# Performance work log

Measured on AMD Instinct MI355X. Metric: run time of the kernel, lower is better.

## Reference

```python
import jax, jax.numpy as jnp
import numpy as np

B, P, IN_DIM, OUT_DIM = 4, 120000, 4, 64
SPATIAL = (480, 360, 32)
EPS = 1e-5
SLOPE = 0.01  # LeakyReLU default negative slope


def setup_inputs() -> dict:
    key = jax.random.key(0)
    ks = jax.random.split(key, 10)
    pc = jax.random.normal(ks[0], (B, P, IN_DIM), dtype=jnp.float32)
    pc_indices = jax.random.randint(ks[1], (B, P, 3), 0, 32, dtype=jnp.int32)
    W1 = jax.random.normal(ks[2], (IN_DIM, 16), dtype=jnp.float32) * (1.0 / np.sqrt(IN_DIM))
    b1 = jax.random.normal(ks[3], (16,), dtype=jnp.float32) * 0.01
    g1 = jnp.ones((16,), jnp.float32)
    be1 = jnp.zeros((16,), jnp.float32)
    W2 = jax.random.normal(ks[4], (16, OUT_DIM), dtype=jnp.float32) * 0.25
    b2 = jax.random.normal(ks[5], (OUT_DIM,), dtype=jnp.float32) * 0.01
    g2 = jnp.ones((OUT_DIM,), jnp.float32)
    be2 = jnp.zeros((OUT_DIM,), jnp.float32)
    return {"pc": pc, "pc_indices": pc_indices, "W1": W1, "b1": b1, "g1": g1,
            "be1": be1, "W2": W2, "b2": b2, "g2": g2, "be2": be2}


def _bn_lrelu(h, g, b):
    # BatchNorm1d in training mode: batch mean / biased variance over points
    mean = jnp.mean(h, axis=0)
    var = jnp.mean((h - mean) ** 2, axis=0)
    h = (h - mean) / jnp.sqrt(var + EPS) * g + b
    return jnp.where(h >= 0, h, SLOPE * h)


def reference(pc, pc_indices, W1, b1, g1, be1, W2, b2, g2, be2):
    N = B * P
    x = pc.reshape(N, IN_DIM)
    bid = jnp.repeat(jnp.arange(B, dtype=jnp.int32), P)  # batch id padded in front
    coords = jnp.concatenate([bid[:, None], pc_indices.reshape(N, 3)], axis=1)  # [N,4]

    # small MLP (shuffle/recover in the original is a mathematical no-op for outputs)
    h = _bn_lrelu(x @ W1 + b1, g1, be1)
    feat = _bn_lrelu(h @ W2 + b2, g2, be2)  # [N, OUT_DIM]

    # torch.unique(dim=0) == lexicographic sort of linearized voxel keys
    S0, S1, S2 = SPATIAL
    key = (((coords[:, 0] * S0 + coords[:, 1]) * S1 + coords[:, 2]) * S2 + coords[:, 3])
    order = jnp.argsort(key)
    sk = key[order]
    is_first = jnp.concatenate([jnp.ones((1,), bool), sk[1:] != sk[:-1]])
    seg_sorted = (jnp.cumsum(is_first) - 1).astype(jnp.int32)  # segment id per sorted point
    inv = jnp.zeros((N,), jnp.int32).at[order].set(seg_sorted)  # inverse index (unsorted)

    # scatter_max into (padded, fixed-shape) voxel feature table
    voxel_feat = jax.ops.segment_max(feat, inv, num_segments=N)  # [N, OUT_DIM]
    n_uni = seg_sorted[-1] + 1
    valid = jnp.arange(N) < n_uni
    voxel_feat = jnp.where(valid[:, None], voxel_feat, 0.0)
    voxel_ind = jnp.zeros((N, 4), jnp.int32).at[seg_sorted].set(coords[order])

    return voxel_feat, voxel_ind, feat
```

## Files before the change

### kernel.cpp

```cpp
#include <hip/hip_runtime.h>

typedef unsigned int u32;
typedef unsigned long long u64;

#define N_PTS 480000
#define PPB   120000
#define NKEY  131072
#define NBLK_A 256
#define NBLK_B 256
#define NT64   7500
#define SLOPE 0.01f

__device__ __forceinline__ u32 bf16pack(float lo, float hi) {
    u32 a = __float_as_uint(lo), b = __float_as_uint(hi);
    a += 0x7fffu + ((a >> 16) & 1u);
    b += 0x7fffu + ((b >> 16) & 1u);
    return (a >> 16) | (b & 0xffff0000u);
}
__device__ __forceinline__ float bf_lo(u32 v) { return __uint_as_float(v << 16); }
__device__ __forceinline__ float bf_hi(u32 v) { return __uint_as_float(v & 0xffff0000u); }

__global__ __launch_bounds__(256) void kZ(u32* __restrict__ cnt) {
    uint4 z; z.x = 0u; z.y = 0u; z.z = 0u; z.w = 0u;
    ((uint4*)cnt)[blockIdx.x * 256 + threadIdx.x] = z;
}

__global__ __launch_bounds__(256) void kA(const float* __restrict__ pc,
                                          const int* __restrict__ pidx,
                                          u32* __restrict__ keys,
                                          u32* __restrict__ cnt,
                                          float* __restrict__ pA) {
    int t = threadIdx.x;
    float a[14];
#pragma unroll
    for (int j = 0; j < 14; ++j) a[j] = 0.f;

    for (int n = blockIdx.x * 256 + t; n < N_PTS; n += gridDim.x * 256) {
        float4 x = ((const float4*)pc)[n];
        a[0] += x.x; a[1] += x.y; a[2] += x.z; a[3] += x.w;
        a[4] += x.x * x.x; a[5] += x.x * x.y; a[6]  += x.x * x.z; a[7]  += x.x * x.w;
        a[8] += x.y * x.y; a[9] += x.y * x.z; a[10] += x.y * x.w;
        a[11] += x.z * x.z; a[12] += x.z * x.w; a[13] += x.w * x.w;

        int i0 = pidx[3 * n], i1 = pidx[3 * n + 1], i2 = pidx[3 * n + 2];
        int bid = n / PPB;
        u32 key = (u32)(bid * 32768 + i0 * 1024 + i1 * 32 + i2);
        keys[n] = key;
        atomicAdd(&cnt[key], 1u);
    }

    __shared__ float red[256];
    for (int j = 0; j < 14; ++j) {
        red[t] = a[j];
        __syncthreads();
        for (int s = 128; s > 0; s >>= 1) {
            if (t < s) red[t] += red[t + s];
            __syncthreads();
        }
        if (t == 0) pA[j * NBLK_A + blockIdx.x] = red[0];
        __syncthreads();
    }
}

__global__ __launch_bounds__(1024) void kR1(const float* __restrict__ pA,
                                            const float* __restrict__ W1,
                                            const float* __restrict__ b1,
                                            const float* __restrict__ g1,
                                            const float* __restrict__ be1,
                                            float* __restrict__ stats1) {
    int t = threadIdx.x, w = t >> 6, lane = t & 63;
    __shared__ float S[14];
    if (w < 14) {
        const float* p = pA + w * NBLK_A;
        float s = p[lane] + p[lane + 64] + p[lane + 128] + p[lane + 192];
        for (int d = 32; d > 0; d >>= 1) s += __shfl_xor(s, d);
        if (lane == 0) S[w] = s;
    }
    __syncthreads();
    if (t < 16) {
        int c = t;
        double w4[4];
#pragma unroll
        for (int i = 0; i < 4; ++i) w4[i] = W1[i * 16 + c];
        double sx[4] = { S[0], S[1], S[2], S[3] };
        auto sxx = [&](int i, int j) -> double {
            if (i > j) { int k = i; i = j; j = k; }
            int base = (i == 0) ? 4 : (i == 1) ? 8 : (i == 2) ? 11 : 13;
            return (double)S[base + (j - i)];
        };
        double su = 0.0;
        for (int i = 0; i < 4; ++i) su += sx[i] * w4[i];
        double q = 0.0;
        for (int i = 0; i < 4; ++i)
            for (int j = 0; j < 4; ++j) q += w4[i] * w4[j] * sxx(i, j);
        double b = (double)b1[c];
        double sum   = su + b * (double)N_PTS;
        double sumsq = q + 2.0 * b * su + (double)N_PTS * b * b;
        double mean = sum / (double)N_PTS;
        double var  = sumsq / (double)N_PTS - mean * mean;
        float inv = rsqrtf((float)(var + 1e-5));
        float sc = g1[c] * inv;
        float sf = be1[c] - (float)mean * sc;
#pragma unroll
        for (int i = 0; i < 4; ++i) stats1[c * 4 + i] = W1[i * 16 + c] * sc;
        stats1[64 + c] = b1[c] * sc + sf;
    }
}

__global__ __launch_bounds__(256, 1) void kB(const float* __restrict__ pc,
                                             const float* __restrict__ stats1,
                                             float* __restrict__ pB) {
    int t = threadIdx.x, w = t >> 6, lane = t & 63;
    __shared__ float sW[80];
    __shared__ float sred[4][152];
    if (t < 80) sW[t] = stats1[t];
    __syncthreads();

    float acc[152];
#pragma unroll
    for (int m = 0; m < 152; ++m) acc[m] = 0.f;

    const float4* sW4 = (const float4*)sW;
    for (int n = blockIdx.x * 256 + t; n < N_PTS; n += NBLK_B * 256) {
        float4 x = ((const float4*)pc)[n];
        float h[16];
#pragma unroll
        for (int k = 0; k < 16; ++k) {
            float4 wk = sW4[k];
            float z = x.x * wk.x + x.y * wk.y + x.z * wk.z + x.w * wk.w + sW[64 + k];
            h[k] = (z >= 0.f) ? z : SLOPE * z;
        }
#pragma unroll
        for (int i = 0; i < 16; ++i) acc[i] += h[i];
#pragma unroll
        for (int i = 0; i < 16; ++i)
#pragma unroll
            for (int j = i; j < 16; ++j)
                acc[16 + i * 16 - (i * (i - 1)) / 2 + (j - i)] += h[i] * h[j];
    }

#pragma unroll
    for (int m = 0; m < 152; ++m) {
        float s = acc[m];
        for (int d = 32; d > 0; d >>= 1) s += __shfl_xor(s, d);
        acc[m] = s;
    }
    if (lane == 0) {
#pragma unroll
        for (int m = 0; m < 152; ++m) sred[w][m] = acc[m];
    }
    __syncthreads();
    if (t < 152)
        pB[t * NBLK_B + blockIdx.x] = sred[0][t] + sred[1][t] + sred[2][t] + sred[3][t];
}

__global__ __launch_bounds__(1024) void kR2(const float* __restrict__ pB,
                                            const float* __restrict__ W2,
                                            const float* __restrict__ b2,
                                            const float* __restrict__ g2,
                                            const float* __restrict__ be2,
                                            float* __restrict__ stats2) {
    int t = threadIdx.x, w = t >> 6, lane = t & 63;
    __shared__ float S[152];
    for (int q = w; q < 152; q += 16) {
        const float* p = pB + q * NBLK_B;
        float s = p[lane] + p[lane + 64] + p[lane + 128] + p[lane + 192];
        for (int d = 32; d > 0; d >>= 1) s += __shfl_xor(s, d);
        if (lane == 0) S[q] = s;
    }
    __syncthreads();
    if (t < 64) {
        double wv[16];
#pragma unroll
        for (int k = 0; k < 16; ++k) wv[k] = W2[k * 64 + t];
        double sh = 0.0;
        for (int k = 0; k < 16; ++k) sh += wv[k] * (double)S[k];
        auto qidx = [&](int i, int j) { return 16 + i * 16 - (i * (i - 1)) / 2 + (j - i); };
        double q = 0.0;
        for (int i = 0; i < 16; ++i) {
            q += wv[i] * wv[i] * (double)S[qidx(i, i)];
            double t2 = 0.0;
            for (int j = i + 1; j < 16; ++j) t2 += wv[j] * (double)S[qidx(i, j)];
            q += 2.0 * wv[i] * t2;
        }
        double b = (double)b2[t];
        double sum   = sh + b * (double)N_PTS;
        double sumsq = q + 2.0 * b * sh + (double)N_PTS * b * b;
        double mean = sum / (double)N_PTS;
        double var  = sumsq / (double)N_PTS - mean * mean;
        float inv = rsqrtf((float)(var + 1e-5));
        float sc = g2[t] * inv;
        float sf = be2[t] - (float)mean * sc;
#pragma unroll
        for (int k = 0; k < 16; ++k) stats2[k * 64 + t] = W2[k * 64 + t] * sc;
        stats2[1024 + t] = b2[t] * sc + sf;
    }
}

__global__ __launch_bounds__(256) void kS1(const u32* __restrict__ cnt,
                                           u32* __restrict__ bsum) {
    int t = threadIdx.x, b = blockIdx.x;
    uint4 c4 = ((const uint4*)cnt)[b * 256 + t];
    u32 cs = c4.x + c4.y + c4.z + c4.w;
    u32 os = (c4.x > 0) + (c4.y > 0) + (c4.z > 0) + (c4.w > 0);
    __shared__ u32 rc[256], ro[256];
    rc[t] = cs; ro[t] = os;
    __syncthreads();
    for (int s = 128; s > 0; s >>= 1) {
        if (t < s) { rc[t] += rc[t + s]; ro[t] += ro[t + s]; }
        __syncthreads();
    }
    if (t == 0) { bsum[2 * b] = rc[0]; bsum[2 * b + 1] = ro[0]; }
}

__global__ __launch_bounds__(256) void kS2(u32* __restrict__ cnt,
                                           const u32* __restrict__ bsum,
                                           u32* __restrict__ startc,
                                           float* __restrict__ vi,
                                           u32* __restrict__ nuni) {
    int t = threadIdx.x, b = blockIdx.x;
    __shared__ u32 sbc[128], sbo[128];
    __shared__ u32 cOff, oOff;
    __shared__ u64 scan[256];
    if (t < 128) { sbc[t] = bsum[2 * t]; sbo[t] = bsum[2 * t + 1]; }

    uint4 c4 = ((const uint4*)cnt)[b * 256 + t];
    u32 cv[4] = { c4.x, c4.y, c4.z, c4.w };
    u32 cs = cv[0] + cv[1] + cv[2] + cv[3];
    u32 os = (cv[0] > 0) + (cv[1] > 0) + (cv[2] > 0) + (cv[3] > 0);
    scan[t] = ((u64)cs << 32) | (u64)os;
    __syncthreads();
    if (t == 0) {
        u32 a = 0, o = 0;
        for (int i = 0; i < b; ++i) { a += sbc[i]; o += sbo[i]; }
        cOff = a; oOff = o;
    }
    for (int d = 1; d < 256; d <<= 1) {
        u64 v = (t >= d) ? scan[t - d] : 0ull;
        __syncthreads();
        scan[t] += v;
        __syncthreads();
    }
    u64 ex = scan[t] - (((u64)cs << 32) | (u64)os);
    u32 start = cOff + (u32)(ex >> 32);
    u32 rank  = oOff + (u32)(ex & 0xffffffffull);

    int kbase = b * 1024 + t * 4;
#pragma unroll
    for (int j = 0; j < 4; ++j) {
        u32 k = (u32)(kbase + j);
        cnt[k] = start;
        if (cv[j] > 0) {
            startc[rank] = start;
            float4 o;
            o.x = (float)(k >> 15);
            o.y = (float)((k >> 10) & 31);
            o.z = (float)((k >> 5) & 31);
            o.w = (float)(k & 31);
            ((float4*)vi)[rank] = o;
            rank++;
        }
        start += cv[j];
    }
    if (b == 127 && t == 255) {
        nuni[0] = rank;
        startc[rank] = N_PTS;
    }
}

__global__ __launch_bounds__(256) void kP(const u32* __restrict__ keys,
                                          u32* __restrict__ cursor,
                                          u32* __restrict__ pid) {
    int n = blockIdx.x * 256 + threadIdx.x;
    if (n < N_PTS) {
        u32 k = keys[n];
        u32 pos = atomicAdd(&cursor[k], 1u);
        pid[pos] = (u32)n;
    }
}

__global__ __launch_bounds__(256) void kC(const float* __restrict__ pc,
                                          const float* __restrict__ stats1,
                                          const float* __restrict__ stats2,
                                          float* __restrict__ feat_out) {
    int t = threadIdx.x;
    __shared__ u32 shp[64][8];

    int cpair = t & 7, psub = t >> 3;
    float w1a[4], w1b[4], c1a, c1b;
#pragma unroll
    for (int i = 0; i < 4; ++i) {
        w1a[i] = stats1[(2 * cpair) * 4 + i];
        w1b[i] = stats1[(2 * cpair + 1) * 4 + i];
    }
    c1a = stats1[64 + 2 * cpair];
    c1b = stats1[64 + 2 * cpair + 1];

    int c2 = t & 63, pg = t >> 6;
    float w2c[16];
#pragma unroll
    for (int k = 0; k < 16; ++k) w2c[k] = stats2[k * 64 + c2];
    float c2fr = stats2[1024 + c2];

    for (int tile = blockIdx.x; tile < NT64; tile += gridDim.x) {
        int base = tile * 64;
#pragma unroll
        for (int half = 0; half < 2; ++half) {
            int p = psub + 32 * half;
            float4 x = ((const float4*)pc)[base + p];
            float za = x.x * w1a[0] + x.y * w1a[1] + x.z * w1a[2] + x.w * w1a[3] + c1a;
            float zb = x.x * w1b[0] + x.y * w1b[1] + x.z * w1b[2] + x.w * w1b[3] + c1b;
            za = (za >= 0.f) ? za : SLOPE * za;
            zb = (zb >= 0.f) ? zb : SLOPE * zb;
            shp[p][cpair] = bf16pack(za, zb);
        }
        __syncthreads();
#pragma unroll
        for (int j = 0; j < 16; ++j) {
            int p = pg + 4 * j;
            const uint4* row = (const uint4*)&shp[p][0];
            uint4 v0 = row[0], v1 = row[1];
            float f = c2fr;
            f += bf_lo(v0.x) * w2c[0]  + bf_hi(v0.x) * w2c[1];
            f += bf_lo(v0.y) * w2c[2]  + bf_hi(v0.y) * w2c[3];
            f += bf_lo(v0.z) * w2c[4]  + bf_hi(v0.z) * w2c[5];
            f += bf_lo(v0.w) * w2c[6]  + bf_hi(v0.w) * w2c[7];
            f += bf_lo(v1.x) * w2c[8]  + bf_hi(v1.x) * w2c[9];
            f += bf_lo(v1.y) * w2c[10] + bf_hi(v1.y) * w2c[11];
            f += bf_lo(v1.z) * w2c[12] + bf_hi(v1.z) * w2c[13];
            f += bf_lo(v1.w) * w2c[14] + bf_hi(v1.w) * w2c[15];
            float ff = (f >= 0.f) ? f : SLOPE * f;
            feat_out[(size_t)(base + p) * 64 + c2] = ff;
        }
        __syncthreads();
    }
}

__global__ __launch_bounds__(256) void kV(const float* __restrict__ feat,
                                          const u32* __restrict__ pid,
                                          const u32* __restrict__ startc,
                                          const u32* __restrict__ nuni,
                                          float* __restrict__ vf,
                                          float* __restrict__ vi) {
    u32 nu = *nuni;
    u32 r0 = blockIdx.x * 4;
    int w = threadIdx.x >> 6, lane = threadIdx.x & 63;

    if (threadIdx.x < 16) {
        u32 row = r0 + (threadIdx.x >> 2);
        if (row >= nu) vi[(size_t)row * 4 + (threadIdx.x & 3)] = 0.f;
    }

    u32 r = r0 + (u32)w;
    if (r < nu) {
        u32 s = startc[r], e = startc[r + 1];
        float m = -3.4e38f;
        for (u32 i = s; i < e; ++i) {
            u32 p = pid[i];
            m = fmaxf(m, feat[(size_t)p * 64 + lane]);
        }
        vf[(size_t)r * 64 + lane] = m;
    } else {
        vf[(size_t)r * 64 + lane] = 0.f;
    }
}

extern "C" void kernel_launch(void* const* d_in, const int* in_sizes, int n_in,
                              void* d_out, int out_size, void* d_ws, size_t ws_size,
                              hipStream_t stream) {
    const float* pc   = (const float*)d_in[0];
    const int*   pidx = (const int*)d_in[1];
    const float* W1   = (const float*)d_in[2];
    const float* b1   = (const float*)d_in[3];
    const float* g1   = (const float*)d_in[4];
    const float* be1  = (const float*)d_in[5];
    const float* W2   = (const float*)d_in[6];
    const float* b2   = (const float*)d_in[7];
    const float* g2   = (const float*)d_in[8];
    const float* be2  = (const float*)d_in[9];

    float* vf   = (float*)d_out;
    float* vi   = vf + (size_t)N_PTS * 64;
    float* feat = vi + (size_t)N_PTS * 4;

    u32* ws     = (u32*)d_ws;
    u32* keys   = ws;
    u32* cnt    = ws + 480000;
    u32* startc = ws + 611072;
    u32* bsum   = ws + 742148;
    u32* nuni   = ws + 742404;
    u32* pid    = ws + 742420;
    float* pA     = (float*)(ws + 1222420);
    float* stats1 = (float*)(ws + 1226004);
    float* pB     = (float*)(ws + 1226084);
    float* stats2 = (float*)(ws + 1264996);

    kZ<<<128, 256, 0, stream>>>(cnt);
    kA<<<NBLK_A, 256, 0, stream>>>(pc, pidx, keys, cnt, pA);
    kR1<<<1, 1024, 0, stream>>>(pA, W1, b1, g1, be1, stats1);
    kB<<<NBLK_B, 256, 0, stream>>>(pc, stats1, pB);
    kR2<<<1, 1024, 0, stream>>>(pB, W2, b2, g2, be2, stats2);
    kS1<<<128, 256, 0, stream>>>(cnt, bsum);
    kS2<<<128, 256, 0, stream>>>(cnt, bsum, startc, vi, nuni);
    kP<<<1875, 256, 0, stream>>>(keys, cnt, pid);
    kC<<<2048, 256, 0, stream>>>(pc, stats1, stats2, feat);
    kV<<<120000, 256, 0, stream>>>(feat, pid, startc, nuni, vf, vi);
}
```

Baseline: 204.9 us.

## Fuse pipeline into five kernels and move the voxel scan into one block

The launch sequence is cut from ten kernels to five. Zeroing of the count table moves into the first stats kernel, and the voxel-count atomics plus the layer-1 BN finalisation move into kB. The layer-2 stats reduction and the whole count scan (formerly two kernels) become one 1024-thread single-block kernel, and the pid scatter is folded into the feature kernel. kV becomes grid-stride with 2048 blocks. This removes launch and inter-kernel gaps, but the scan now runs serially on one CU with strided per-thread reads, and every kB block redundantly recomputes stats1.

```diff
diff --git a/kernel.cpp b/kernel.cpp
--- a/kernel.cpp
+++ b/kernel.cpp
@@ -20,22 +20,20 @@
 __device__ __forceinline__ float bf_lo(u32 v) { return __uint_as_float(v << 16); }
 __device__ __forceinline__ float bf_hi(u32 v) { return __uint_as_float(v & 0xffff0000u); }
 
-__global__ __launch_bounds__(256) void kZ(u32* __restrict__ cnt) {
-    uint4 z; z.x = 0u; z.y = 0u; z.z = 0u; z.w = 0u;
-    ((uint4*)cnt)[blockIdx.x * 256 + threadIdx.x] = z;
-}
-
-__global__ __launch_bounds__(256) void kA(const float* __restrict__ pc,
-                                          const int* __restrict__ pidx,
-                                          u32* __restrict__ keys,
-                                          u32* __restrict__ cnt,
-                                          float* __restrict__ pA) {
+__global__ __launch_bounds__(256) void kA0(const float* __restrict__ pc,
+                                           const int* __restrict__ pidx,
+                                           u32* __restrict__ keys,
+                                           u32* __restrict__ cnt,
+                                           float* __restrict__ pA) {
     int t = threadIdx.x;
+    int g = blockIdx.x * 256 + t;
+    ((u64*)cnt)[g] = 0ull;
+
     float a[14];
 #pragma unroll
     for (int j = 0; j < 14; ++j) a[j] = 0.f;
 
-    for (int n = blockIdx.x * 256 + t; n < N_PTS; n += gridDim.x * 256) {
+    for (int n = g; n < N_PTS; n += NBLK_A * 256) {
         float4 x = ((const float4*)pc)[n];
         a[0] += x.x; a[1] += x.y; a[2] += x.z; a[3] += x.w;
         a[4] += x.x * x.x; a[5] += x.x * x.y; a[6]  += x.x * x.z; a[7]  += x.x * x.w;
@@ -44,9 +42,7 @@
 
         int i0 = pidx[3 * n], i1 = pidx[3 * n + 1], i2 = pidx[3 * n + 2];
         int bid = n / PPB;
-        u32 key = (u32)(bid * 32768 + i0 * 1024 + i1 * 32 + i2);
-        keys[n] = key;
-        atomicAdd(&cnt[key], 1u);
+        keys[n] = (u32)(bid * 32768 + i0 * 1024 + i1 * 32 + i2);
     }
 
     __shared__ float red[256];
@@ -62,19 +58,26 @@
     }
 }
 
-__global__ __launch_bounds__(1024) void kR1(const float* __restrict__ pA,
-                                            const float* __restrict__ W1,
-                                            const float* __restrict__ b1,
-                                            const float* __restrict__ g1,
-                                            const float* __restrict__ be1,
-                                            float* __restrict__ stats1) {
+__global__ __launch_bounds__(256, 1) void kB(const float* __restrict__ pc,
+                                             const u32* __restrict__ keys,
+                                             const float* __restrict__ pA,
+                                             const float* __restrict__ W1,
+                                             const float* __restrict__ b1,
+                                             const float* __restrict__ g1,
+                                             const float* __restrict__ be1,
+                                             u32* __restrict__ cnt,
+                                             float* __restrict__ pB,
+                                             float* __restrict__ stats1) {
     int t = threadIdx.x, w = t >> 6, lane = t & 63;
     __shared__ float S[14];
-    if (w < 14) {
-        const float* p = pA + w * NBLK_A;
+    __shared__ float sW[80];
+    __shared__ float sred[4][152];
+
+    for (int q = w; q < 14; q += 4) {
+        const float* p = pA + q * NBLK_A;
         float s = p[lane] + p[lane + 64] + p[lane + 128] + p[lane + 192];
         for (int d = 32; d > 0; d >>= 1) s += __shfl_xor(s, d);
-        if (lane == 0) S[w] = s;
+        if (lane == 0) S[q] = s;
     }
     __syncthreads();
     if (t < 16) {
@@ -102,19 +105,18 @@
         float sc = g1[c] * inv;
         float sf = be1[c] - (float)mean * sc;
 #pragma unroll
-        for (int i = 0; i < 4; ++i) stats1[c * 4 + i] = W1[i * 16 + c] * sc;
-        stats1[64 + c] = b1[c] * sc + sf;
-    }
-}
-
-__global__ __launch_bounds__(256, 1) void kB(const float* __restrict__ pc,
-                                             const float* __restrict__ stats1,
-                                             float* __restrict__ pB) {
-    int t = threadIdx.x, w = t >> 6, lane = t & 63;
-    __shared__ float sW[80];
-    __shared__ float sred[4][152];
-    if (t < 80) sW[t] = stats1[t];
-    __syncthreads();
+        for (int i = 0; i < 4; ++i) sW[c * 4 + i] = W1[i * 16 + c] * sc;
+        sW[64 + c] = b1[c] * sc + sf;
+        if (blockIdx.x == 0) {
+#pragma unroll
+            for (int i = 0; i < 4; ++i) stats1[c * 4 + i] = sW[c * 4 + i];
+            stats1[64 + c] = sW[64 + c];
+        }
+    }
+    __syncthreads();
+
+    for (int n = blockIdx.x * 256 + t; n < N_PTS; n += NBLK_B * 256)
+        atomicAdd(&cnt[keys[n]], 1u);
 
     float acc[152];
 #pragma unroll
@@ -154,14 +156,20 @@
         pB[t * NBLK_B + blockIdx.x] = sred[0][t] + sred[1][t] + sred[2][t] + sred[3][t];
 }
 
-__global__ __launch_bounds__(1024) void kR2(const float* __restrict__ pB,
-                                            const float* __restrict__ W2,
-                                            const float* __restrict__ b2,
-                                            const float* __restrict__ g2,
-                                            const float* __restrict__ be2,
-                                            float* __restrict__ stats2) {
+__global__ __launch_bounds__(1024) void kMid(const float* __restrict__ pB,
+                                             const float* __restrict__ W2,
+                                             const float* __restrict__ b2,
+                                             const float* __restrict__ g2,
+                                             const float* __restrict__ be2,
+                                             float* __restrict__ stats2,
+                                             u32* cnt,
+                                             u32* __restrict__ startc,
+                                             float* __restrict__ vi,
+                                             u32* __restrict__ nuni) {
     int t = threadIdx.x, w = t >> 6, lane = t & 63;
     __shared__ float S[152];
+    __shared__ u64 sc[1024];
+
     for (int q = w; q < 152; q += 16) {
         const float* p = pB + q * NBLK_B;
         float s = p[lane] + p[lane + 64] + p[lane + 128] + p[lane + 192];
@@ -189,101 +197,77 @@
         double mean = sum / (double)N_PTS;
         double var  = sumsq / (double)N_PTS - mean * mean;
         float inv = rsqrtf((float)(var + 1e-5));
-        float sc = g2[t] * inv;
-        float sf = be2[t] - (float)mean * sc;
-#pragma unroll
-        for (int k = 0; k < 16; ++k) stats2[k * 64 + t] = W2[k * 64 + t] * sc;
-        stats2[1024 + t] = b2[t] * sc + sf;
-    }
-}
-
-__global__ __launch_bounds__(256) void kS1(const u32* __restrict__ cnt,
-                                           u32* __restrict__ bsum) {
-    int t = threadIdx.x, b = blockIdx.x;
-    uint4 c4 = ((const uint4*)cnt)[b * 256 + t];
-    u32 cs = c4.x + c4.y + c4.z + c4.w;
-    u32 os = (c4.x > 0) + (c4.y > 0) + (c4.z > 0) + (c4.w > 0);
-    __shared__ u32 rc[256], ro[256];
-    rc[t] = cs; ro[t] = os;
-    __syncthreads();
-    for (int s = 128; s > 0; s >>= 1) {
-        if (t < s) { rc[t] += rc[t + s]; ro[t] += ro[t + s]; }
-        __syncthreads();
-    }
-    if (t == 0) { bsum[2 * b] = rc[0]; bsum[2 * b + 1] = ro[0]; }
-}
-
-__global__ __launch_bounds__(256) void kS2(u32* __restrict__ cnt,
-                                           const u32* __restrict__ bsum,
-                                           u32* __restrict__ startc,
-                                           float* __restrict__ vi,
-                                           u32* __restrict__ nuni) {
-    int t = threadIdx.x, b = blockIdx.x;
-    __shared__ u32 sbc[128], sbo[128];
-    __shared__ u32 cOff, oOff;
-    __shared__ u64 scan[256];
-    if (t < 128) { sbc[t] = bsum[2 * t]; sbo[t] = bsum[2 * t + 1]; }
-
-    uint4 c4 = ((const uint4*)cnt)[b * 256 + t];
-    u32 cv[4] = { c4.x, c4.y, c4.z, c4.w };
-    u32 cs = cv[0] + cv[1] + cv[2] + cv[3];
-    u32 os = (cv[0] > 0) + (cv[1] > 0) + (cv[2] > 0) + (cv[3] > 0);
-    scan[t] = ((u64)cs << 32) | (u64)os;
-    __syncthreads();
-    if (t == 0) {
-        u32 a = 0, o = 0;
-        for (int i = 0; i < b; ++i) { a += sbc[i]; o += sbo[i]; }
-        cOff = a; oOff = o;
-    }
-    for (int d = 1; d < 256; d <<= 1) {
-        u64 v = (t >= d) ? scan[t - d] : 0ull;
-        __syncthreads();
-        scan[t] += v;
-        __syncthreads();
-    }
-    u64 ex = scan[t] - (((u64)cs << 32) | (u64)os);
-    u32 start = cOff + (u32)(ex >> 32);
-    u32 rank  = oOff + (u32)(ex & 0xffffffffull);
-
-    int kbase = b * 1024 + t * 4;
-#pragma unroll
-    for (int j = 0; j < 4; ++j) {
-        u32 k = (u32)(kbase + j);
-        cnt[k] = start;
-        if (cv[j] > 0) {
-            startc[rank] = start;
-            float4 o;
-            o.x = (float)(k >> 15);
-            o.y = (float)((k >> 10) & 31);
-            o.z = (float)((k >> 5) & 31);
-            o.w = (float)(k & 31);
-            ((float4*)vi)[rank] = o;
-            rank++;
-        }
-        start += cv[j];
-    }
-    if (b == 127 && t == 255) {
+        float scs = g2[t] * inv;
+        float sf = be2[t] - (float)mean * scs;
+#pragma unroll
+        for (int k = 0; k < 16; ++k) stats2[k * 64 + t] = W2[k * 64 + t] * scs;
+        stats2[1024 + t] = b2[t] * scs + sf;
+    }
+    __syncthreads();
+
+    const uint4* c4 = (const uint4*)cnt;
+    int base4 = t * 32;
+    u32 ls = 0, lo = 0;
+    for (int j = 0; j < 32; ++j) {
+        uint4 v = c4[base4 + j];
+        ls += v.x + v.y + v.z + v.w;
+        lo += (v.x > 0) + (v.y > 0) + (v.z > 0) + (v.w > 0);
+    }
+    u64 mine = ((u64)ls << 32) | (u64)lo;
+    sc[t] = mine;
+    __syncthreads();
+    for (int d = 1; d < 1024; d <<= 1) {
+        u64 v = (t >= d) ? sc[t - d] : 0ull;
+        __syncthreads();
+        sc[t] += v;
+        __syncthreads();
+    }
+    u64 ex = sc[t] - mine;
+    u32 start = (u32)(ex >> 32);
+    u32 rank  = (u32)(ex & 0xffffffffull);
+
+    for (int j = 0; j < 32; ++j) {
+        uint4 v = c4[base4 + j];
+        u32 k0 = (u32)(base4 + j) * 4;
+        u32 cv[4] = { v.x, v.y, v.z, v.w };
+#pragma unroll
+        for (int e = 0; e < 4; ++e) {
+            u32 k = k0 + e;
+            cnt[k] = start;
+            if (cv[e] > 0) {
+                startc[rank] = start;
+                float4 o;
+                o.x = (float)(k >> 15);
+                o.y = (float)((k >> 10) & 31);
+                o.z = (float)((k >> 5) & 31);
+                o.w = (float)(k & 31);
+                ((float4*)vi)[rank] = o;
+                rank++;
+            }
+            start += cv[e];
+        }
+    }
+    if (t == 1023) {
         nuni[0] = rank;
         startc[rank] = N_PTS;
     }
 }
 
-__global__ __launch_bounds__(256) void kP(const u32* __restrict__ keys,
+__global__ __launch_bounds__(256) void kC(const float* __restrict__ pc,
+                                          const u32* __restrict__ keys,
                                           u32* __restrict__ cursor,
-                                          u32* __restrict__ pid) {
-    int n = blockIdx.x * 256 + threadIdx.x;
-    if (n < N_PTS) {
-        u32 k = keys[n];
-        u32 pos = atomicAdd(&cursor[k], 1u);
-        pid[pos] = (u32)n;
-    }
-}
-
-__global__ __launch_bounds__(256) void kC(const float* __restrict__ pc,
+                                          u32* __restrict__ pid,
                                           const float* __restrict__ stats1,
                                           const float* __restrict__ stats2,
                                           float* __restrict__ feat_out) {
     int t = threadIdx.x;
+
+    for (int n = blockIdx.x * 256 + t; n < N_PTS; n += 2048 * 256) {
+        u32 k = keys[n];
+        u32 pos = atomicAdd(&cursor[k], 1u);
+        pid[pos] = (u32)n;
+    }
+
     __shared__ u32 shp[64][8];
 
     int cpair = t & 7, psub = t >> 3;
@@ -302,7 +286,7 @@
     for (int k = 0; k < 16; ++k) w2c[k] = stats2[k * 64 + c2];
     float c2fr = stats2[1024 + c2];
 
-    for (int tile = blockIdx.x; tile < NT64; tile += gridDim.x) {
+    for (int tile = blockIdx.x; tile < NT64; tile += 2048) {
         int base = tile * 64;
 #pragma unroll
         for (int half = 0; half < 2; ++half) {
@@ -343,25 +327,20 @@
                                           float* __restrict__ vf,
                                           float* __restrict__ vi) {
     u32 nu = *nuni;
-    u32 r0 = blockIdx.x * 4;
     int w = threadIdx.x >> 6, lane = threadIdx.x & 63;
-
-    if (threadIdx.x < 16) {
-        u32 row = r0 + (threadIdx.x >> 2);
-        if (row >= nu) vi[(size_t)row * 4 + (threadIdx.x & 3)] = 0.f;
-    }
-
-    u32 r = r0 + (u32)w;
-    if (r < nu) {
-        u32 s = startc[r], e = startc[r + 1];
-        float m = -3.4e38f;
-        for (u32 i = s; i < e; ++i) {
-            u32 p = pid[i];
-            m = fmaxf(m, feat[(size_t)p * 64 + lane]);
-        }
-        vf[(size_t)r * 64 + lane] = m;
-    } else {
-        vf[(size_t)r * 64 + lane] = 0.f;
+    for (u32 r = blockIdx.x * 4 + (u32)w; r < N_PTS; r += 8192) {
+        if (r < nu) {
+            u32 s = startc[r], e = startc[r + 1];
+            float m = -3.4e38f;
+            for (u32 i = s; i < e; ++i) {
+                u32 p = pid[i];
+                m = fmaxf(m, feat[(size_t)p * 64 + lane]);
+            }
+            vf[(size_t)r * 64 + lane] = m;
+        } else {
+            vf[(size_t)r * 64 + lane] = 0.f;
+            if (lane < 4) vi[(size_t)r * 4 + lane] = 0.f;
+        }
     }
 }
 
@@ -387,22 +366,16 @@
     u32* keys   = ws;
     u32* cnt    = ws + 480000;
     u32* startc = ws + 611072;
-    u32* bsum   = ws + 742148;
-    u32* nuni   = ws + 742404;
-    u32* pid    = ws + 742420;
-    float* pA     = (float*)(ws + 1222420);
-    float* stats1 = (float*)(ws + 1226004);
-    float* pB     = (float*)(ws + 1226084);
-    float* stats2 = (float*)(ws + 1264996);
-
-    kZ<<<128, 256, 0, stream>>>(cnt);
-    kA<<<NBLK_A, 256, 0, stream>>>(pc, pidx, keys, cnt, pA);
-    kR1<<<1, 1024, 0, stream>>>(pA, W1, b1, g1, be1, stats1);
-    kB<<<NBLK_B, 256, 0, stream>>>(pc, stats1, pB);
-    kR2<<<1, 1024, 0, stream>>>(pB, W2, b2, g2, be2, stats2);
-    kS1<<<128, 256, 0, stream>>>(cnt, bsum);
-    kS2<<<128, 256, 0, stream>>>(cnt, bsum, startc, vi, nuni);
-    kP<<<1875, 256, 0, stream>>>(keys, cnt, pid);
-    kC<<<2048, 256, 0, stream>>>(pc, stats1, stats2, feat);
-    kV<<<120000, 256, 0, stream>>>(feat, pid, startc, nuni, vf, vi);
-}
+    u32* nuni   = ws + 742148;
+    u32* pid    = ws + 742164;
+    float* pA     = (float*)(ws + 1222164);
+    float* stats1 = (float*)(ws + 1225748);
+    float* pB     = (float*)(ws + 1225828);
+    float* stats2 = (float*)(ws + 1264740);
+
+    kA0<<<NBLK_A, 256, 0, stream>>>(pc, pidx, keys, cnt, pA);
+    kB<<<NBLK_B, 256, 0, stream>>>(pc, keys, pA, W1, b1, g1, be1, cnt, pB, stats1);
+    kMid<<<1, 1024, 0, stream>>>(pB, W2, b2, g2, be2, stats2, cnt, startc, vi, nuni);
+    kC<<<2048, 256, 0, stream>>>(pc, keys, cnt, pid, stats1, stats2, feat);
+    kV<<<2048, 256, 0, stream>>>(feat, pid, startc, nuni, vf, vi);
+}
```

Measured after the change: 415.7 us. +102.9%, slower.

## Merge small stat/zero/scatter kernels into neighbours and persist voxel kernel

Applied to the files above, without the earlier changes.

Cuts the launch count from ten to six. Zeroing of the count table moves into the first kernel, and the layer-1 stats reduction is recomputed redundantly in every block of kB. The count atomics move into kB, the layer-2 stats are folded into block 0 of kS1, and point-id placement is fused into kC. The voxel max kernel becomes a grid-stride loop over 2048 blocks instead of 120000. The aim is to remove launch overhead and the single-block serial kernels, at the cost of redundant per-block work and a longer serial tail in kS1's block 0.

```diff
diff --git a/kernel.cpp b/kernel.cpp
--- a/kernel.cpp
+++ b/kernel.cpp
@@ -20,22 +20,20 @@
 __device__ __forceinline__ float bf_lo(u32 v) { return __uint_as_float(v << 16); }
 __device__ __forceinline__ float bf_hi(u32 v) { return __uint_as_float(v & 0xffff0000u); }
 
-__global__ __launch_bounds__(256) void kZ(u32* __restrict__ cnt) {
-    uint4 z; z.x = 0u; z.y = 0u; z.z = 0u; z.w = 0u;
-    ((uint4*)cnt)[blockIdx.x * 256 + threadIdx.x] = z;
-}
-
-__global__ __launch_bounds__(256) void kA(const float* __restrict__ pc,
-                                          const int* __restrict__ pidx,
-                                          u32* __restrict__ keys,
-                                          u32* __restrict__ cnt,
-                                          float* __restrict__ pA) {
+__global__ __launch_bounds__(256) void kA0(const float* __restrict__ pc,
+                                           const int* __restrict__ pidx,
+                                           u32* __restrict__ keys,
+                                           u32* __restrict__ cnt,
+                                           float* __restrict__ pA) {
     int t = threadIdx.x;
+    int g = blockIdx.x * 256 + t;
+    ((u64*)cnt)[g] = 0ull;
+
     float a[14];
 #pragma unroll
     for (int j = 0; j < 14; ++j) a[j] = 0.f;
 
-    for (int n = blockIdx.x * 256 + t; n < N_PTS; n += gridDim.x * 256) {
+    for (int n = g; n < N_PTS; n += NBLK_A * 256) {
         float4 x = ((const float4*)pc)[n];
         a[0] += x.x; a[1] += x.y; a[2] += x.z; a[3] += x.w;
         a[4] += x.x * x.x; a[5] += x.x * x.y; a[6]  += x.x * x.z; a[7]  += x.x * x.w;
@@ -44,9 +42,7 @@
 
         int i0 = pidx[3 * n], i1 = pidx[3 * n + 1], i2 = pidx[3 * n + 2];
         int bid = n / PPB;
-        u32 key = (u32)(bid * 32768 + i0 * 1024 + i1 * 32 + i2);
-        keys[n] = key;
-        atomicAdd(&cnt[key], 1u);
+        keys[n] = (u32)(bid * 32768 + i0 * 1024 + i1 * 32 + i2);
     }
 
     __shared__ float red[256];
@@ -62,19 +58,26 @@
     }
 }
 
-__global__ __launch_bounds__(1024) void kR1(const float* __restrict__ pA,
-                                            const float* __restrict__ W1,
-                                            const float* __restrict__ b1,
-                                            const float* __restrict__ g1,
-                                            const float* __restrict__ be1,
-                                            float* __restrict__ stats1) {
+__global__ __launch_bounds__(256, 1) void kB(const float* __restrict__ pc,
+                                             const u32* __restrict__ keys,
+                                             const float* __restrict__ pA,
+                                             const float* __restrict__ W1,
+                                             const float* __restrict__ b1,
+                                             const float* __restrict__ g1,
+                                             const float* __restrict__ be1,
+                                             u32* __restrict__ cnt,
+                                             float* __restrict__ pB,
+                                             float* __restrict__ stats1) {
     int t = threadIdx.x, w = t >> 6, lane = t & 63;
     __shared__ float S[14];
-    if (w < 14) {
-        const float* p = pA + w * NBLK_A;
+    __shared__ float sW[80];
+    __shared__ float sred[4][152];
+
+    for (int q = w; q < 14; q += 4) {
+        const float* p = pA + q * NBLK_A;
         float s = p[lane] + p[lane + 64] + p[lane + 128] + p[lane + 192];
         for (int d = 32; d > 0; d >>= 1) s += __shfl_xor(s, d);
-        if (lane == 0) S[w] = s;
+        if (lane == 0) S[q] = s;
     }
     __syncthreads();
     if (t < 16) {
@@ -102,19 +105,18 @@
         float sc = g1[c] * inv;
         float sf = be1[c] - (float)mean * sc;
 #pragma unroll
-        for (int i = 0; i < 4; ++i) stats1[c * 4 + i] = W1[i * 16 + c] * sc;
-        stats1[64 + c] = b1[c] * sc + sf;
-    }
-}
-
-__global__ __launch_bounds__(256, 1) void kB(const float* __restrict__ pc,
-                                             const float* __restrict__ stats1,
-                                             float* __restrict__ pB) {
-    int t = threadIdx.x, w = t >> 6, lane = t & 63;
-    __shared__ float sW[80];
-    __shared__ float sred[4][152];
-    if (t < 80) sW[t] = stats1[t];
+        for (int i = 0; i < 4; ++i) sW[c * 4 + i] = W1[i * 16 + c] * sc;
+        sW[64 + c] = b1[c] * sc + sf;
+        if (blockIdx.x == 0) {
+#pragma unroll
+            for (int i = 0; i < 4; ++i) stats1[c * 4 + i] = sW[c * 4 + i];
+            stats1[64 + c] = sW[64 + c];
+        }
+    }
     __syncthreads();
+
+    for (int n = blockIdx.x * 256 + t; n < N_PTS; n += NBLK_B * 256)
+        atomicAdd(&cnt[keys[n]], 1u);
 
     float acc[152];
 #pragma unroll
@@ -154,51 +156,14 @@
         pB[t * NBLK_B + blockIdx.x] = sred[0][t] + sred[1][t] + sred[2][t] + sred[3][t];
 }
 
-__global__ __launch_bounds__(1024) void kR2(const float* __restrict__ pB,
-                                            const float* __restrict__ W2,
-                                            const float* __restrict__ b2,
-                                            const float* __restrict__ g2,
-                                            const float* __restrict__ be2,
-                                            float* __restrict__ stats2) {
-    int t = threadIdx.x, w = t >> 6, lane = t & 63;
-    __shared__ float S[152];
-    for (int q = w; q < 152; q += 16) {
-        const float* p = pB + q * NBLK_B;
-        float s = p[lane] + p[lane + 64] + p[lane + 128] + p[lane + 192];
-        for (int d = 32; d > 0; d >>= 1) s += __shfl_xor(s, d);
-        if (lane == 0) S[q] = s;
-    }
-    __syncthreads();
-    if (t < 64) {
-        double wv[16];
-#pragma unroll
-        for (int k = 0; k < 16; ++k) wv[k] = W2[k * 64 + t];
-        double sh = 0.0;
-        for (int k = 0; k < 16; ++k) sh += wv[k] * (double)S[k];
-        auto qidx = [&](int i, int j) { return 16 + i * 16 - (i * (i - 1)) / 2 + (j - i); };
-        double q = 0.0;
-        for (int i = 0; i < 16; ++i) {
-            q += wv[i] * wv[i] * (double)S[qidx(i, i)];
-            double t2 = 0.0;
-            for (int j = i + 1; j < 16; ++j) t2 += wv[j] * (double)S[qidx(i, j)];
-            q += 2.0 * wv[i] * t2;
-        }
-        double b = (double)b2[t];
-        double sum   = sh + b * (double)N_PTS;
-        double sumsq = q + 2.0 * b * sh + (double)N_PTS * b * b;
-        double mean = sum / (double)N_PTS;
-        double var  = sumsq / (double)N_PTS - mean * mean;
-        float inv = rsqrtf((float)(var + 1e-5));
-        float sc = g2[t] * inv;
-        float sf = be2[t] - (float)mean * sc;
-#pragma unroll
-        for (int k = 0; k < 16; ++k) stats2[k * 64 + t] = W2[k * 64 + t] * sc;
-        stats2[1024 + t] = b2[t] * sc + sf;
-    }
-}
-
 __global__ __launch_bounds__(256) void kS1(const u32* __restrict__ cnt,
-                                           u32* __restrict__ bsum) {
+                                           u32* __restrict__ bsum,
+                                           const float* __restrict__ pB,
+                                           const float* __restrict__ W2,
+                                           const float* __restrict__ b2,
+                                           const float* __restrict__ g2,
+                                           const float* __restrict__ be2,
+                                           float* __restrict__ stats2) {
     int t = threadIdx.x, b = blockIdx.x;
     uint4 c4 = ((const uint4*)cnt)[b * 256 + t];
     u32 cs = c4.x + c4.y + c4.z + c4.w;
@@ -211,6 +176,44 @@
         __syncthreads();
     }
     if (t == 0) { bsum[2 * b] = rc[0]; bsum[2 * b + 1] = ro[0]; }
+
+    if (b == 0) {
+        int w = t >> 6, lane = t & 63;
+        __shared__ float S[152];
+        for (int q = w; q < 152; q += 4) {
+            const float* p = pB + q * NBLK_B;
+            float s = p[lane] + p[lane + 64] + p[lane + 128] + p[lane + 192];
+            for (int d = 32; d > 0; d >>= 1) s += __shfl_xor(s, d);
+            if (lane == 0) S[q] = s;
+        }
+        __syncthreads();
+        if (t < 64) {
+            double wv[16];
+#pragma unroll
+            for (int k = 0; k < 16; ++k) wv[k] = W2[k * 64 + t];
+            double sh = 0.0;
+            for (int k = 0; k < 16; ++k) sh += wv[k] * (double)S[k];
+            auto qidx = [&](int i, int j) { return 16 + i * 16 - (i * (i - 1)) / 2 + (j - i); };
+            double q = 0.0;
+            for (int i = 0; i < 16; ++i) {
+                q += wv[i] * wv[i] * (double)S[qidx(i, i)];
+                double t2 = 0.0;
+                for (int j = i + 1; j < 16; ++j) t2 += wv[j] * (double)S[qidx(i, j)];
+                q += 2.0 * wv[i] * t2;
+            }
+            double bb = (double)b2[t];
+            double sum   = sh + bb * (double)N_PTS;
+            double sumsq = q + 2.0 * bb * sh + (double)N_PTS * bb * bb;
+            double mean = sum / (double)N_PTS;
+            double var  = sumsq / (double)N_PTS - mean * mean;
+            float inv = rsqrtf((float)(var + 1e-5));
+            float scs = g2[t] * inv;
+            float sf = be2[t] - (float)mean * scs;
+#pragma unroll
+            for (int k = 0; k < 16; ++k) stats2[k * 64 + t] = W2[k * 64 + t] * scs;
+            stats2[1024 + t] = b2[t] * scs + sf;
+        }
+    }
 }
 
 __global__ __launch_bounds__(256) void kS2(u32* __restrict__ cnt,
@@ -268,22 +271,21 @@
     }
 }
 
-__global__ __launch_bounds__(256) void kP(const u32* __restrict__ keys,
+__global__ __launch_bounds__(256) void kC(const float* __restrict__ pc,
+                                          const u32* __restrict__ keys,
                                           u32* __restrict__ cursor,
-                                          u32* __restrict__ pid) {
-    int n = blockIdx.x * 256 + threadIdx.x;
-    if (n < N_PTS) {
-        u32 k = keys[n];
-        u32 pos = atomicAdd(&cursor[k], 1u);
-        pid[pos] = (u32)n;
-    }
-}
-
-__global__ __launch_bounds__(256) void kC(const float* __restrict__ pc,
+                                          u32* __restrict__ pid,
                                           const float* __restrict__ stats1,
                                           const float* __restrict__ stats2,
                                           float* __restrict__ feat_out) {
     int t = threadIdx.x;
+
+    for (int n = blockIdx.x * 256 + t; n < N_PTS; n += 2048 * 256) {
+        u32 k = keys[n];
+        u32 pos = atomicAdd(&cursor[k], 1u);
+        pid[pos] = (u32)n;
+    }
+
     __shared__ u32 shp[64][8];
 
     int cpair = t & 7, psub = t >> 3;
@@ -302,7 +304,7 @@
     for (int k = 0; k < 16; ++k) w2c[k] = stats2[k * 64 + c2];
     float c2fr = stats2[1024 + c2];
 
-    for (int tile = blockIdx.x; tile < NT64; tile += gridDim.x) {
+    for (int tile = blockIdx.x; tile < NT64; tile += 2048) {
         int base = tile * 64;
 #pragma unroll
         for (int half = 0; half < 2; ++half) {
@@ -343,25 +345,20 @@
                                           float* __restrict__ vf,
                                           float* __restrict__ vi) {
     u32 nu = *nuni;
-    u32 r0 = blockIdx.x * 4;
     int w = threadIdx.x >> 6, lane = threadIdx.x & 63;
-
-    if (threadIdx.x < 16) {
-        u32 row = r0 + (threadIdx.x >> 2);
-        if (row >= nu) vi[(size_t)row * 4 + (threadIdx.x & 3)] = 0.f;
-    }
-
-    u32 r = r0 + (u32)w;
-    if (r < nu) {
-        u32 s = startc[r], e = startc[r + 1];
-        float m = -3.4e38f;
-        for (u32 i = s; i < e; ++i) {
-            u32 p = pid[i];
-            m = fmaxf(m, feat[(size_t)p * 64 + lane]);
-        }
-        vf[(size_t)r * 64 + lane] = m;
-    } else {
-        vf[(size_t)r * 64 + lane] = 0.f;
+    for (u32 r = blockIdx.x * 4 + (u32)w; r < N_PTS; r += 8192) {
+        if (r < nu) {
+            u32 s = startc[r], e = startc[r + 1];
+            float m = -3.4e38f;
+            for (u32 i = s; i < e; ++i) {
+                u32 p = pid[i];
+                m = fmaxf(m, feat[(size_t)p * 64 + lane]);
+            }
+            vf[(size_t)r * 64 + lane] = m;
+        } else {
+            vf[(size_t)r * 64 + lane] = 0.f;
+            if (lane < 4) vi[(size_t)r * 4 + lane] = 0.f;
+        }
     }
 }
 
@@ -395,14 +392,10 @@
     float* pB     = (float*)(ws + 1226084);
     float* stats2 = (float*)(ws + 1264996);
 
-    kZ<<<128, 256, 0, stream>>>(cnt);
-    kA<<<NBLK_A, 256, 0, stream>>>(pc, pidx, keys, cnt, pA);
-    kR1<<<1, 1024, 0, stream>>>(pA, W1, b1, g1, be1, stats1);
-    kB<<<NBLK_B, 256, 0, stream>>>(pc, stats1, pB);
-    kR2<<<1, 1024, 0, stream>>>(pB, W2, b2, g2, be2, stats2);
-    kS1<<<128, 256, 0, stream>>>(cnt, bsum);
+    kA0<<<NBLK_A, 256, 0, stream>>>(pc, pidx, keys, cnt, pA);
+    kB<<<NBLK_B, 256, 0, stream>>>(pc, keys, pA, W1, b1, g1, be1, cnt, pB, stats1);
+    kS1<<<128, 256, 0, stream>>>(cnt, bsum, pB, W2, b2, g2, be2, stats2);
     kS2<<<128, 256, 0, stream>>>(cnt, bsum, startc, vi, nuni);
-    kP<<<1875, 256, 0, stream>>>(keys, cnt, pid);
-    kC<<<2048, 256, 0, stream>>>(pc, stats1, stats2, feat);
-    kV<<<120000, 256, 0, stream>>>(feat, pid, startc, nuni, vf, vi);
-}
+    kC<<<2048, 256, 0, stream>>>(pc, keys, cnt, pid, stats1, stats2, feat);
+    kV<<<2048, 256, 0, stream>>>(feat, pid, startc, nuni, vf, vi);
+}
```

After: 195.6 us. 4.6% less time.
